# Optimization experiments

Measured on AMD Instinct MI355X. Metric: run time of the kernel, lower is better.

Reference implementation:

```python
import jax, jax.numpy as jnp
import numpy as np

B, S, DIM = 2, 4096, 1024
H, HD = 16, 64          # num_heads, head_dim (DIM = H*HD)
KN = 64                 # k neighbors per query
SCALE = 1.0 / np.sqrt(HD)
CANTOR_DEPTH = 8


def _cantor_coords(seq_len: int, depth: int = CANTOR_DEPTH) -> np.ndarray:
    """Vectorized replica of CantorAttention._compute_cantor_coord."""
    x = np.arange(seq_len, dtype=np.float64) / max(1, seq_len - 1)
    x = np.clip(x, 1e-06, 1.0 - 1e-06)
    val = np.zeros(seq_len, dtype=np.float64)
    factor = 0.5
    for _ in range(depth):
        xs = x * 3.0
        digit = np.floor(xs)
        x = xs - digit
        val += factor * (digit == 2)
        factor *= 0.5
    return val.astype(np.float32)


def _build_routes(seq_len: int, k: int) -> np.ndarray:
    coords = _cantor_coords(seq_len)
    dist = np.abs(coords[:, None] - coords[None, :])  # [S, S]
    routes = np.argsort(dist, axis=1, kind='stable')[:, :k]  # k smallest
    return routes.astype(np.int32)


def setup_inputs() -> dict:
    key = jax.random.key(0)
    kx, kw1, kb1, kw2, kb2 = jax.random.split(key, 5)
    x = jax.random.normal(kx, (B, S, DIM), dtype=jnp.float32)
    # learned params (qkv and out projections)
    W_qkv = jax.random.normal(kw1, (DIM, 3 * DIM), dtype=jnp.float32) * (1.0 / np.sqrt(DIM))
    b_qkv = jax.random.normal(kb1, (3 * DIM,), dtype=jnp.float32) * 0.01
    W_out = jax.random.normal(kw2, (DIM, DIM), dtype=jnp.float32) * (1.0 / np.sqrt(DIM))
    b_out = jax.random.normal(kb2, (DIM,), dtype=jnp.float32) * 0.01
    routes = jnp.asarray(_build_routes(S, KN))  # [S, KN] int32, positional Cantor kNN
    return {"x": x, "W_qkv": W_qkv, "b_qkv": b_qkv, "W_out": W_out, "b_out": b_out, "routes": routes}


def reference(x, W_qkv, b_qkv, W_out, b_out, routes):
    Bs, Sl, _ = x.shape
    qkv = x @ W_qkv + b_qkv                                   # [B,S,3*DIM]
    qkv = qkv.reshape(Bs, Sl, 3, H, HD).transpose(2, 0, 3, 1, 4)
    q, k, v = qkv[0], qkv[1], qkv[2]                          # [B,H,S,HD]
    k_g = k[:, :, routes, :]                                  # [B,H,S,KN,HD]
    v_g = v[:, :, routes, :]                                  # [B,H,S,KN,HD]
    scores = jnp.einsum('bhqd,bhqkd->bhqk', q, k_g) * SCALE   # [B,H,S,KN]
    attn = jax.nn.softmax(scores, axis=-1)
    out = jnp.einsum('bhqk,bhqkd->bhqd', attn, v_g)           # [B,H,S,HD]
    out = out.transpose(0, 2, 1, 3).reshape(Bs, Sl, DIM)
    return out @ W_out + b_out
```

## Files before the change

### kernel.cpp

```cpp
#include <hip/hip_runtime.h>
#include <hip/hip_bf16.h>
#include <stdint.h>

#define DEVI __device__ __forceinline__

typedef __bf16 bf16x8 __attribute__((ext_vector_type(8)));
typedef float f32x4 __attribute__((ext_vector_type(4)));
typedef unsigned short ushort8v __attribute__((ext_vector_type(8)));

static constexpr int SEQ = 4096;
static constexpr int DIM_ = 1024;
static constexpr int NH = 16;
static constexpr int HD_ = 64;
static constexpr float SCALE_ = 0.125f;

DEVI unsigned short f2bf(float f) {
  __hip_bfloat16 h = __float2bfloat16(f);
  return __builtin_bit_cast(unsigned short, h);
}


__global__ void k_cvt_bf16(const float* __restrict__ in, unsigned short* __restrict__ out) {
  int i = (blockIdx.x * 256 + threadIdx.x) * 4;
  float4 v = *reinterpret_cast<const float4*>(in + i);
  ushort4 o;
  o.x = f2bf(v.x); o.y = f2bf(v.y); o.z = f2bf(v.z); o.w = f2bf(v.w);
  *reinterpret_cast<ushort4*>(out + i) = o;
}

__global__ void k_transpose_cvt(const float* __restrict__ in, unsigned short* __restrict__ out,
                                int K, int N) {
  __shared__ float tile[64][65];
  const int n0 = blockIdx.x * 64, k0 = blockIdx.y * 64;
  const int tr = threadIdx.x >> 6, tc = threadIdx.x & 63;
#pragma unroll
  for (int p = 0; p < 16; ++p) {
    int r = p * 4 + tr;
    tile[r][tc] = in[(size_t)(k0 + r) * N + n0 + tc];
  }
  __syncthreads();
#pragma unroll
  for (int p = 0; p < 16; ++p) {
    int r = p * 4 + tr;
    out[(size_t)(n0 + r) * K + k0 + tc] = f2bf(tile[tc][r]);
  }
}


DEVI void load16_lds(const void* g, void* l) {
  __builtin_amdgcn_global_load_lds((__attribute__((address_space(1))) void*)(g),
                                   (__attribute__((address_space(3))) void*)(l),
                                   16, 0, 0);
}

template <int MODE>
__global__ __launch_bounds__(256, 4)
void k_gemm_bt(const unsigned short* __restrict__ A,
               const unsigned short* __restrict__ Bt,
               const float* __restrict__ bias,
               float* __restrict__ outF,
               unsigned short* __restrict__ outQ,
               unsigned short* __restrict__ outK,
               unsigned short* __restrict__ outV,
               int M, int N, int K) {
  constexpr int BK = 32;
  __shared__ alignas(16) unsigned short As[128 * BK];
  __shared__ alignas(16) unsigned short Bs[128 * BK];
  const int tid = threadIdx.x;
  const int wave = tid >> 6, lane = tid & 63;
  const int wr = wave >> 1, wc = wave & 1;
  const int l15 = lane & 15, q = lane >> 4;

  const int gm = M >> 7;
  const int nwg = gm * (N >> 7);
  int wg = blockIdx.y * gridDim.x + blockIdx.x;
  wg = (wg & 7) * (nwg >> 3) + (wg >> 3);
  const int bm = (wg % gm) * 128;
  const int bn = (wg / gm) * 128;

  f32x4 acc[4][4] = {};

  const int srow = lane >> 2;
  const int scol = ((lane & 3) ^ ((lane >> 3) & 3)) * 8;
  const unsigned short* aS0 = A + (size_t)(bm + wave * 16 + srow) * K + scol;
  const unsigned short* aS1 = aS0 + (size_t)64 * K;
  const unsigned short* bS0 = Bt + (size_t)(bn + wave * 16 + srow) * K + scol;
  const unsigned short* bS1 = bS0 + (size_t)64 * K;
  unsigned short* aD0 = &As[(wave * 16) * BK];
  unsigned short* aD1 = &As[(64 + wave * 16) * BK];
  unsigned short* bD0 = &Bs[(wave * 16) * BK];
  unsigned short* bD1 = &Bs[(64 + wave * 16) * BK];

  const int x3 = (l15 >> 1) & 3;
  const unsigned short* aRd = &As[(wr * 64 + l15) * BK + (q ^ x3) * 8];
  const unsigned short* bRd = &Bs[(wc * 64 + l15) * BK + (q ^ x3) * 8];

  for (int k0 = 0; k0 < K; k0 += BK) {
    load16_lds(aS0 + k0, aD0);
    load16_lds(aS1 + k0, aD1);
    load16_lds(bS0 + k0, bD0);
    load16_lds(bS1 + k0, bD1);
    __syncthreads();

    bf16x8 af[4], bfr[4];
#pragma unroll
    for (int m = 0; m < 4; ++m)
      af[m] = *reinterpret_cast<const bf16x8*>(aRd + m * 16 * BK);
#pragma unroll
    for (int n = 0; n < 4; ++n)
      bfr[n] = *reinterpret_cast<const bf16x8*>(bRd + n * 16 * BK);
#pragma unroll
    for (int m = 0; m < 4; ++m)
#pragma unroll
      for (int n = 0; n < 4; ++n)
        acc[m][n] = __builtin_amdgcn_mfma_f32_16x16x32_bf16(af[m], bfr[n], acc[m][n], 0, 0, 0);
    __syncthreads();
  }

  const int r0 = q * 4;
#pragma unroll
  for (int m = 0; m < 4; ++m) {
#pragma unroll
    for (int n = 0; n < 4; ++n) {
      const int col = bn + wc * 64 + n * 16 + l15;
      const float bv = bias[col];
#pragma unroll
      for (int j = 0; j < 4; ++j) {
        const int row = bm + wr * 64 + m * 16 + r0 + j;
        const float v = acc[m][n][j] + bv;
        if constexpr (MODE == 0) {
          outF[(size_t)row * N + col] = v;
        } else {
          const int t = col >> 10;
          const int hh = (col >> 6) & 15;
          const int d = col & 63;
          const int b = row >> 12;
          const int s = row & 4095;
          unsigned short* dst = (t == 0) ? outQ : (t == 1) ? outK : outV;
          dst[((size_t)(b * NH + hh) * SEQ + s) * HD_ + d] = f2bf(v);
        }
      }
    }
  }
}


__global__ void k_gid(const int* __restrict__ routes, int* __restrict__ gid, int* __restrict__ cnt) {
  const int s = blockIdx.x * 256 + threadIdx.x;
  const int lead = routes[s * 64];
  int g = s;
  if (lead >= 0 && lead < SEQ && lead != s) {
    bool eq = true;
    const int4* a = reinterpret_cast<const int4*>(routes + (size_t)s * 64);
    const int4* b = reinterpret_cast<const int4*>(routes + (size_t)lead * 64);
#pragma unroll
    for (int i = 0; i < 16; ++i) {
      int4 x = a[i], y = b[i];
      eq = eq && (x.x == y.x) && (x.y == y.y) && (x.z == y.z) && (x.w == y.w);
    }
    if (eq) g = lead;
  }
  gid[s] = g;
  atomicAdd(&cnt[g], 1);
}

__global__ void k_tilebase(const int* __restrict__ cnt, int* __restrict__ tileBase,
                           int* __restrict__ nTiles) {
  const int g = blockIdx.x * 256 + threadIdx.x;
  const int c = cnt[g];
  if (c > 0) {
    tileBase[g] = atomicAdd(nTiles, (c + 15) >> 4);
  }
}

__global__ void k_scatter(const int* __restrict__ gid, const int* __restrict__ tileBase,
                          int* __restrict__ pos, int* __restrict__ tileQ,
                          int* __restrict__ tileLead) {
  const int s = blockIdx.x * 256 + threadIdx.x;
  const int g = gid[s];
  const int p = atomicAdd(&pos[g], 1);
  const int tile = tileBase[g] + (p >> 4);
  tileQ[tile * 16 + (p & 15)] = s;
  if ((p & 15) == 0) tileLead[tile] = g;
}


__global__ __launch_bounds__(256)
void k_attn_grp(const unsigned short* __restrict__ Q,
                const unsigned short* __restrict__ Kb,
                const unsigned short* __restrict__ Vb,
                const int* __restrict__ routes,
                const int* __restrict__ tileQ,
                const int* __restrict__ tileLead,
                const int* __restrict__ nTilesPtr,
                unsigned short* __restrict__ att) {
  const int nT = *nTilesPtr;

  __shared__ int sMemRaw[16];
  __shared__ int sMemEff[16];
  __shared__ int sRoutes[64];
  __shared__ alignas(16) unsigned short sKV[4][4096];
  __shared__ alignas(16) unsigned short sP[4][16 * 72];

  const int tid = threadIdx.x;
  const int wave = tid >> 6, lane = tid & 63;
  unsigned short* KV = sKV[wave];
  unsigned short* P = sP[wave];
  const int hi = lane >> 4;
  const int l15 = lane & 15;
  const int l7 = lane & 7;
  const int rr = lane >> 3;

  for (int tile = blockIdx.x; tile < nT; tile += gridDim.x) {
    __syncthreads();
    if (tid < 16) {
      const int v = tileQ[tile * 16 + tid];
      const int v0 = tileQ[tile * 16];
      sMemRaw[tid] = v;
      sMemEff[tid] = (v < 0) ? v0 : v;
    } else if (tid >= 64 && tid < 128) {
      const int lead = tileLead[tile];
      sRoutes[tid - 64] = routes[(size_t)lead * 64 + (tid - 64)];
    }
    __syncthreads();

#pragma unroll 1
    for (int ih = 0; ih < 2; ++ih) {
      const int bh = blockIdx.y * 8 + wave * 2 + ih;
      const size_t base = (size_t)bh * (SEQ * HD_);

      __builtin_amdgcn_s_waitcnt(0);
      __builtin_amdgcn_sched_barrier(0);

      {
        const int sc = ((l7 - rr) & 7) * 8;
#pragma unroll
        for (int t = 0; t < 8; ++t) {
          const int rk = sRoutes[t * 8 + rr];
          load16_lds(Kb + base + (size_t)rk * HD_ + sc, &KV[t * 512]);
        }
      }

      bf16x8 qa0, qa1;
      {
        const unsigned short* qrow = Q + base + (size_t)sMemEff[l15] * HD_ + hi * 8;
        qa0 = *reinterpret_cast<const bf16x8*>(qrow);
        qa1 = *reinterpret_cast<const bf16x8*>(qrow + 32);
      }
      __builtin_amdgcn_s_waitcnt(0);
      __builtin_amdgcn_sched_barrier(0);

      f32x4 accS[4] = {};
#pragma unroll
      for (int nb = 0; nb < 4; ++nb) {
        const int key = nb * 16 + l15;
        const int rot = 8 * (key & 7);
        const int ae0 = key * 64 + (((hi * 8) + rot) & 63);
        const int ae1 = key * 64 + (((32 + hi * 8) + rot) & 63);
        bf16x8 kf0 = *reinterpret_cast<const bf16x8*>(&KV[ae0]);
        bf16x8 kf1 = *reinterpret_cast<const bf16x8*>(&KV[ae1]);
        accS[nb] = __builtin_amdgcn_mfma_f32_16x16x32_bf16(qa0, kf0, accS[nb], 0, 0, 0);
        accS[nb] = __builtin_amdgcn_mfma_f32_16x16x32_bf16(qa1, kf1, accS[nb], 0, 0, 0);
      }

#pragma unroll
      for (int jj = 0; jj < 4; ++jj) {
        float m = fmaxf(fmaxf(accS[0][jj], accS[1][jj]), fmaxf(accS[2][jj], accS[3][jj]));
#pragma unroll
        for (int o = 1; o < 16; o <<= 1) m = fmaxf(m, __shfl_xor(m, o));
        const float e0 = __expf((accS[0][jj] - m) * SCALE_);
        const float e1 = __expf((accS[1][jj] - m) * SCALE_);
        const float e2 = __expf((accS[2][jj] - m) * SCALE_);
        const float e3 = __expf((accS[3][jj] - m) * SCALE_);
        float sum = (e0 + e1) + (e2 + e3);
#pragma unroll
        for (int o = 1; o < 16; o <<= 1) sum += __shfl_xor(sum, o);
        const float rs = __builtin_amdgcn_rcpf(sum);
        const int row = hi * 4 + jj;
        P[row * 72 + 0 + l15] = f2bf(e0 * rs);
        P[row * 72 + 16 + l15] = f2bf(e1 * rs);
        P[row * 72 + 32 + l15] = f2bf(e2 * rs);
        P[row * 72 + 48 + l15] = f2bf(e3 * rs);
      }

      asm volatile("s_waitcnt lgkmcnt(0)" ::: "memory");
      __builtin_amdgcn_sched_barrier(0);
      {
#pragma unroll
        for (int t = 0; t < 8; ++t) {
          const int rk = sRoutes[t * 8 + rr];
          const int sc = ((l7 - 2 * (t & 3)) & 7) * 8;
          load16_lds(Vb + base + (size_t)rk * HD_ + sc, &KV[t * 512]);
        }
      }
      __builtin_amdgcn_s_waitcnt(0);
      __builtin_amdgcn_sched_barrier(0);

      f32x4 accO[4] = {};
#pragma unroll
      for (int ks = 0; ks < 2; ++ks) {
        bf16x8 pf = *reinterpret_cast<const bf16x8*>(&P[l15 * 72 + ks * 32 + hi * 8]);
#pragma unroll
        for (int nb = 0; nb < 4; ++nb) {
          const int d = nb * 16 + l15;
          const int rot = (d + 16 * hi) & 63;
          bf16x8 vf;
#pragma unroll
          for (int j = 0; j < 8; ++j) {
            const int k = ks * 32 + hi * 8 + j;
            vf[j] = *reinterpret_cast<const __bf16*>(&KV[k * 64 + rot]);
          }
          accO[nb] = __builtin_amdgcn_mfma_f32_16x16x32_bf16(pf, vf, accO[nb], 0, 0, 0);
        }
      }

      const int b = bh >> 4, h = bh & 15;
#pragma unroll
      for (int jj = 0; jj < 4; ++jj) {
        const int sQ = sMemRaw[hi * 4 + jj];
        if (sQ >= 0) {
#pragma unroll
          for (int nb = 0; nb < 4; ++nb) {
            att[((size_t)(b * SEQ + sQ)) * DIM_ + h * HD_ + nb * 16 + l15] = f2bf(accO[nb][jj]);
          }
        }
      }
    }
  }
}


extern "C" void kernel_launch(void* const* d_in, const int* in_sizes, int n_in,
                              void* d_out, int out_size, void* d_ws, size_t ws_size,
                              hipStream_t stream) {
  (void)in_sizes; (void)n_in; (void)out_size; (void)ws_size;
  const float* x      = (const float*)d_in[0];
  const float* Wqkv   = (const float*)d_in[1];
  const float* bqkv   = (const float*)d_in[2];
  const float* Wout   = (const float*)d_in[3];
  const float* bout   = (const float*)d_in[4];
  const int*   routes = (const int*)d_in[5];
  float* out = (float*)d_out;

  uint8_t* ws = (uint8_t*)d_ws;
  unsigned short* wqkvT = (unsigned short*)(ws);
  unsigned short* woutT = (unsigned short*)(ws + 6291456);
  unsigned short* Qb    = (unsigned short*)(ws + 8388608);
  unsigned short* Kb    = (unsigned short*)(ws + 25165824);
  unsigned short* Vb    = (unsigned short*)(ws + 41943040);
  unsigned short* att   = (unsigned short*)(ws + 58720256);

  unsigned short* xb = (unsigned short*)d_out;
  uint8_t* g0 = (uint8_t*)d_out + (16u << 20);
  int* gidArr   = (int*)(g0);
  int* cnt      = (int*)(g0 + 16384);
  int* pos      = (int*)(g0 + 32768);
  int* tileBase = (int*)(g0 + 49152);
  int* nTiles   = (int*)(g0 + 65536);
  int* tileLead = (int*)(g0 + 81920);
  int* tileQ    = (int*)(g0 + 98304);

  hipMemsetAsync(cnt, 0, 16384, stream);
  hipMemsetAsync(pos, 0, 16384, stream);
  hipMemsetAsync(nTiles, 0, 4, stream);
  hipMemsetAsync(tileQ, 0xFF, 4096 * 16 * 4, stream);

  k_gid<<<16, 256, 0, stream>>>(routes, gidArr, cnt);
  k_tilebase<<<16, 256, 0, stream>>>(cnt, tileBase, nTiles);
  k_scatter<<<16, 256, 0, stream>>>(gidArr, tileBase, pos, tileQ, tileLead);

  k_cvt_bf16<<<8192, 256, 0, stream>>>(x, xb);
  k_transpose_cvt<<<dim3(48, 16), 256, 0, stream>>>(Wqkv, wqkvT, 1024, 3072);
  k_transpose_cvt<<<dim3(16, 16), 256, 0, stream>>>(Wout, woutT, 1024, 1024);

  k_gemm_bt<1><<<dim3(64, 24), 256, 0, stream>>>(xb, wqkvT, bqkv, nullptr, Qb, Kb, Vb,
                                                 8192, 3072, 1024);
  k_attn_grp<<<dim3(256, 4), 256, 0, stream>>>(Qb, Kb, Vb, routes, tileQ, tileLead,
                                               nTiles, att);
  k_gemm_bt<0><<<dim3(64, 8), 256, 0, stream>>>(att, woutT, bout, out,
                                                nullptr, nullptr, nullptr, 8192, 1024, 1024);
}
```

Before: 182.2 us.

## Double-buffer GEMM LDS tiles and prefetch V alongside K in attention

The GEMM main loop now uses two LDS buffers and issues the next K-tile's global-to-LDS loads before the current tile's MFMAs, so memory latency overlaps compute. The workgroup swizzle that remapped tiles is replaced by a plain blockIdx mapping, which may change L2 locality. In the attention kernel, K and V get separate LDS buffers and the V gather is issued right after K, with a partial vmcnt wait so the QK^T and softmax overlap the V loads. This doubles LDS use in both kernels, which can lower occupancy.

```diff
diff --git a/kernel.cpp b/kernel.cpp
--- a/kernel.cpp
+++ b/kernel.cpp
@@ -64,19 +64,13 @@
                unsigned short* __restrict__ outV,
                int M, int N, int K) {
   constexpr int BK = 32;
-  __shared__ alignas(16) unsigned short As[128 * BK];
-  __shared__ alignas(16) unsigned short Bs[128 * BK];
+  __shared__ alignas(16) unsigned short As[2][128 * BK];
+  __shared__ alignas(16) unsigned short Bs[2][128 * BK];
   const int tid = threadIdx.x;
   const int wave = tid >> 6, lane = tid & 63;
   const int wr = wave >> 1, wc = wave & 1;
   const int l15 = lane & 15, q = lane >> 4;
-
-  const int gm = M >> 7;
-  const int nwg = gm * (N >> 7);
-  int wg = blockIdx.y * gridDim.x + blockIdx.x;
-  wg = (wg & 7) * (nwg >> 3) + (wg >> 3);
-  const int bm = (wg % gm) * 128;
-  const int bn = (wg / gm) * 128;
+  const int bm = blockIdx.x * 128, bn = blockIdx.y * 128;
 
   f32x4 acc[4][4] = {};
 
@@ -86,34 +80,44 @@
   const unsigned short* aS1 = aS0 + (size_t)64 * K;
   const unsigned short* bS0 = Bt + (size_t)(bn + wave * 16 + srow) * K + scol;
   const unsigned short* bS1 = bS0 + (size_t)64 * K;
-  unsigned short* aD0 = &As[(wave * 16) * BK];
-  unsigned short* aD1 = &As[(64 + wave * 16) * BK];
-  unsigned short* bD0 = &Bs[(wave * 16) * BK];
-  unsigned short* bD1 = &Bs[(64 + wave * 16) * BK];
+  const int dOff = (wave * 16) * BK;
 
   const int x3 = (l15 >> 1) & 3;
-  const unsigned short* aRd = &As[(wr * 64 + l15) * BK + (q ^ x3) * 8];
-  const unsigned short* bRd = &Bs[(wc * 64 + l15) * BK + (q ^ x3) * 8];
-
-  for (int k0 = 0; k0 < K; k0 += BK) {
-    load16_lds(aS0 + k0, aD0);
-    load16_lds(aS1 + k0, aD1);
-    load16_lds(bS0 + k0, bD0);
-    load16_lds(bS1 + k0, bD1);
-    __syncthreads();
+  const int aRdOff = (wr * 64 + l15) * BK + (q ^ x3) * 8;
+  const int bRdOff = (wc * 64 + l15) * BK + (q ^ x3) * 8;
+
+  load16_lds(aS0, &As[0][dOff]);
+  load16_lds(aS1, &As[0][dOff + 64 * BK]);
+  load16_lds(bS0, &Bs[0][dOff]);
+  load16_lds(bS1, &Bs[0][dOff + 64 * BK]);
+  __syncthreads();
+
+  const int NT = K / BK;
+#pragma unroll 1
+  for (int t = 0; t < NT; ++t) {
+    const int cur = t & 1;
+    if (t + 1 < NT) {
+      const int k1 = (t + 1) * BK;
+      const int nxt = cur ^ 1;
+      load16_lds(aS0 + k1, &As[nxt][dOff]);
+      load16_lds(aS1 + k1, &As[nxt][dOff + 64 * BK]);
+      load16_lds(bS0 + k1, &Bs[nxt][dOff]);
+      load16_lds(bS1 + k1, &Bs[nxt][dOff + 64 * BK]);
+    }
 
     bf16x8 af[4], bfr[4];
 #pragma unroll
     for (int m = 0; m < 4; ++m)
-      af[m] = *reinterpret_cast<const bf16x8*>(aRd + m * 16 * BK);
+      af[m] = *reinterpret_cast<const bf16x8*>(&As[cur][aRdOff + m * 16 * BK]);
 #pragma unroll
     for (int n = 0; n < 4; ++n)
-      bfr[n] = *reinterpret_cast<const bf16x8*>(bRd + n * 16 * BK);
+      bfr[n] = *reinterpret_cast<const bf16x8*>(&Bs[cur][bRdOff + n * 16 * BK]);
 #pragma unroll
     for (int m = 0; m < 4; ++m)
 #pragma unroll
       for (int n = 0; n < 4; ++n)
         acc[m][n] = __builtin_amdgcn_mfma_f32_16x16x32_bf16(af[m], bfr[n], acc[m][n], 0, 0, 0);
+
     __syncthreads();
   }
 
@@ -199,12 +203,14 @@
   __shared__ int sMemRaw[16];
   __shared__ int sMemEff[16];
   __shared__ int sRoutes[64];
-  __shared__ alignas(16) unsigned short sKV[4][4096];
+  __shared__ alignas(16) unsigned short sK[4][4096];
+  __shared__ alignas(16) unsigned short sV[4][4096];
   __shared__ alignas(16) unsigned short sP[4][16 * 72];
 
   const int tid = threadIdx.x;
   const int wave = tid >> 6, lane = tid & 63;
-  unsigned short* KV = sKV[wave];
+  unsigned short* KL = sK[wave];
+  unsigned short* VL = sV[wave];
   unsigned short* P = sP[wave];
   const int hi = lane >> 4;
   const int l15 = lane & 15;
@@ -229,25 +235,31 @@
       const int bh = blockIdx.y * 8 + wave * 2 + ih;
       const size_t base = (size_t)bh * (SEQ * HD_);
 
-      __builtin_amdgcn_s_waitcnt(0);
-      __builtin_amdgcn_sched_barrier(0);
-
-      {
-        const int sc = ((l7 - rr) & 7) * 8;
-#pragma unroll
-        for (int t = 0; t < 8; ++t) {
-          const int rk = sRoutes[t * 8 + rr];
-          load16_lds(Kb + base + (size_t)rk * HD_ + sc, &KV[t * 512]);
-        }
-      }
-
       bf16x8 qa0, qa1;
       {
         const unsigned short* qrow = Q + base + (size_t)sMemEff[l15] * HD_ + hi * 8;
         qa0 = *reinterpret_cast<const bf16x8*>(qrow);
         qa1 = *reinterpret_cast<const bf16x8*>(qrow + 32);
       }
-      __builtin_amdgcn_s_waitcnt(0);
+
+      {
+        const int sc = ((l7 - rr) & 7) * 8;
+#pragma unroll
+        for (int t = 0; t < 8; ++t) {
+          const int rk = sRoutes[t * 8 + rr];
+          load16_lds(Kb + base + (size_t)rk * HD_ + sc, &KL[t * 512]);
+        }
+      }
+      {
+#pragma unroll
+        for (int t = 0; t < 8; ++t) {
+          const int rk = sRoutes[t * 8 + rr];
+          const int sc = ((l7 - 2 * (t & 3)) & 7) * 8;
+          load16_lds(Vb + base + (size_t)rk * HD_ + sc, &VL[t * 512]);
+        }
+      }
+
+      asm volatile("s_waitcnt vmcnt(8)" ::: "memory");
       __builtin_amdgcn_sched_barrier(0);
 
       f32x4 accS[4] = {};
@@ -257,8 +269,8 @@
         const int rot = 8 * (key & 7);
         const int ae0 = key * 64 + (((hi * 8) + rot) & 63);
         const int ae1 = key * 64 + (((32 + hi * 8) + rot) & 63);
-        bf16x8 kf0 = *reinterpret_cast<const bf16x8*>(&KV[ae0]);
-        bf16x8 kf1 = *reinterpret_cast<const bf16x8*>(&KV[ae1]);
+        bf16x8 kf0 = *reinterpret_cast<const bf16x8*>(&KL[ae0]);
+        bf16x8 kf1 = *reinterpret_cast<const bf16x8*>(&KL[ae1]);
         accS[nb] = __builtin_amdgcn_mfma_f32_16x16x32_bf16(qa0, kf0, accS[nb], 0, 0, 0);
         accS[nb] = __builtin_amdgcn_mfma_f32_16x16x32_bf16(qa1, kf1, accS[nb], 0, 0, 0);
       }
@@ -283,17 +295,7 @@
         P[row * 72 + 48 + l15] = f2bf(e3 * rs);
       }
 
-      asm volatile("s_waitcnt lgkmcnt(0)" ::: "memory");
-      __builtin_amdgcn_sched_barrier(0);
-      {
-#pragma unroll
-        for (int t = 0; t < 8; ++t) {
-          const int rk = sRoutes[t * 8 + rr];
-          const int sc = ((l7 - 2 * (t & 3)) & 7) * 8;
-          load16_lds(Vb + base + (size_t)rk * HD_ + sc, &KV[t * 512]);
-        }
-      }
-      __builtin_amdgcn_s_waitcnt(0);
+      asm volatile("s_waitcnt vmcnt(0) lgkmcnt(0)" ::: "memory");
       __builtin_amdgcn_sched_barrier(0);
 
       f32x4 accO[4] = {};
@@ -308,7 +310,7 @@
 #pragma unroll
           for (int j = 0; j < 8; ++j) {
             const int k = ks * 32 + hi * 8 + j;
-            vf[j] = *reinterpret_cast<const __bf16*>(&KV[k * 64 + rot]);
+            vf[j] = *reinterpret_cast<const __bf16*>(&VL[k * 64 + rot]);
           }
           accO[nb] = __builtin_amdgcn_mfma_f32_16x16x32_bf16(pf, vf, accO[nb], 0, 0, 0);
         }
```

Measured after the change: 174.0 us. 4.5% less time.
